# Performance work log

Hardware: AMD Instinct MI355X
Metric: run time of the kernel (lower is better)

The kernel has to match this reference:

```python
import jax, jax.numpy as jnp
import numpy as np

T, F, H = 65536, 128, 64

def setup_inputs() -> dict:
    key = jax.random.key(0)
    ks = jax.random.split(key, 16)
    s1 = 1.0 / np.sqrt(H).astype(np.float32)   # torch nn.LSTM init bound (hidden=64)
    s2 = 1.0 / np.sqrt(F).astype(np.float32)   # torch nn.LSTM(feats, feats) / Linear bound
    u = lambda k, shape, s: jax.random.uniform(k, shape, jnp.float32, -s, s)
    return {
        "x": jax.random.normal(ks[0], (T, F), jnp.float32),
        "h1_0": jax.random.uniform(ks[1], (H,), jnp.float32),   # torch.rand
        "c1_0": jax.random.normal(ks[2], (H,), jnp.float32),    # torch.randn
        "h2_0": jax.random.uniform(ks[3], (F,), jnp.float32),
        "c2_0": jax.random.normal(ks[4], (F,), jnp.float32),
        "W_ih1": u(ks[5], (4 * H, F), s1),
        "W_hh1": u(ks[6], (4 * H, H), s1),
        "b_ih1": u(ks[7], (4 * H,), s1),
        "b_hh1": u(ks[8], (4 * H,), s1),
        "W_ih2": u(ks[9], (4 * F, F), s2),
        "W_hh2": u(ks[10], (4 * F, F), s2),
        "b_ih2": u(ks[11], (4 * F,), s2),
        "b_hh2": u(ks[12], (4 * F,), s2),
        "W_fc": u(ks[13], (F, F), s2),
        "b_fc": u(ks[14], (F,), s2),
    }

def _lstm_cell(gates, h, c, W_hh):
    # gates: precomputed x-part [4D]; torch gate order: i, f, g, o
    g = gates + W_hh @ h
    i, f, gg, o = jnp.split(g, 4)
    c_new = jax.nn.sigmoid(f) * c + jax.nn.sigmoid(i) * jnp.tanh(gg)
    h_new = jax.nn.sigmoid(o) * jnp.tanh(c_new)
    return h_new, c_new

def reference(x, h1_0, c1_0, h2_0, c2_0, W_ih1, W_hh1, b_ih1, b_hh1,
              W_ih2, W_hh2, b_ih2, b_hh2, W_fc, b_fc):
    # Hoist all input-to-hidden GEMMs out of the scan (one big matmul each).
    gx1 = x @ W_ih1.T + (b_ih1 + b_hh1)  # [T, 4H]
    gx2 = x @ W_ih2.T + (b_ih2 + b_hh2)  # [T, 4F]

    def step(carry, gs):
        h1, c1, h2, c2 = carry
        g1, g2 = gs
        h1, c1 = _lstm_cell(g1, h1, c1, W_hh1)  # lstm1: state evolves, output unused
        h2, c2 = _lstm_cell(g2, h2, c2, W_hh2)
        out = 2.0 * jax.nn.sigmoid(W_fc @ h2 + b_fc)
        return (h1, c1, h2, c2), out

    _, ys = jax.lax.scan(step, (h1_0, c1_0, h2_0, c2_0), (gx1, gx2))
    return ys  # [T, F]
```

## Files before the change

### kernel.cpp

```cpp
#include <hip/hip_runtime.h>
#include <hip/hip_fp16.h>

#define T_LEN 65536
#define FDIM  128
#define CH    16
#define SEG   256
#define WARM  128
#define NBLK  (T_LEN / SEG)
#define GXT   256
#define FCT   256

typedef int iv4 __attribute__((ext_vector_type(4)));
typedef _Float16 h8f __attribute__((ext_vector_type(8)));
typedef float f4v __attribute__((ext_vector_type(4)));

__device__ __forceinline__ float frcp(float x) { return __builtin_amdgcn_rcpf(x); }
#define LOG2E 1.4426950408889634f
__device__ __forceinline__ float sigmoid_f(float x) {
  return frcp(1.f + __builtin_amdgcn_exp2f(-LOG2E * x));
}

union G2u { uint2 u2; __half h[4]; };

#define LDS_BARRIER() asm volatile("s_waitcnt lgkmcnt(0)\n\ts_barrier" ::: "memory")

__device__ __forceinline__ h8f cvt8(const float4 lo, const float4 hi) {
  h8f f;
  f[0] = (_Float16)lo.x; f[1] = (_Float16)lo.y;
  f[2] = (_Float16)lo.z; f[3] = (_Float16)lo.w;
  f[4] = (_Float16)hi.x; f[5] = (_Float16)hi.y;
  f[6] = (_Float16)hi.z; f[7] = (_Float16)hi.w;
  return f;
}

__global__ __launch_bounds__(256)
void prep_kernel(const float* __restrict__ Whh2, signed char* __restrict__ qW,
                 float* __restrict__ qscale)
{
  const int row = blockIdx.x * 256 + threadIdx.x;
  const float* wr = Whh2 + (size_t)row * FDIM;
  float mjg[4];
#pragma unroll
  for (int jg = 0; jg < 4; ++jg) {
    float m = 0.f;
#pragma unroll
    for (int kc = 0; kc < 2; ++kc)
#pragma unroll
      for (int j = 0; j < 16; ++j)
        m = fmaxf(m, fabsf(wr[16 * jg + 64 * kc + j]));
    mjg[jg] = m;
  }
  float s = fmaxf(fmaxf(mjg[0], mjg[1]), fmaxf(mjg[2], mjg[3]));
  s = fmaxf(s, 1e-20f);
  qscale[row] = s * (1.f / 16129.f);
  const float inv = 127.f / s;
  signed char* qr = qW + (size_t)row * FDIM;
#pragma unroll
  for (int k = 0; k < FDIM; ++k) {
    int qv = (int)rintf(wr[k] * inv);
    qv = qv < -127 ? -127 : (qv > 127 ? 127 : qv);
    qr[k] = (signed char)qv;
  }
}

__global__ __launch_bounds__(256)
void gx_kernel(const float* __restrict__ x, const float* __restrict__ Wih2,
               const float* __restrict__ bih2, const float* __restrict__ bhh2,
               __half* __restrict__ gx)
{
  __shared__ __align__(16) float  xs[16 * 132];
  __shared__ __align__(16) __half gp[4][16 * 130];

  const int tid  = threadIdx.x;
  const int lane = tid & 63;
  const int w    = tid >> 6;
  const int col  = lane & 15;
  const int kg   = lane >> 4;

  h8f  bf[8][4];
  float bias[8];
  const float gmul = (w == 2) ? (-2.f * LOG2E) : (-LOG2E);
#pragma unroll
  for (int nt = 0; nt < 8; ++nt) {
    const int row = w * 128 + nt * 16 + col;
    bias[nt] = bih2[row] + bhh2[row];
    const float* wr = Wih2 + (size_t)row * FDIM + kg * 8;
#pragma unroll
    for (int kc = 0; kc < 4; ++kc)
      bf[nt][kc] = cvt8(*(const float4*)(wr + kc * 32),
                        *(const float4*)(wr + kc * 32 + 4));
  }

  const int tbase = blockIdx.x * GXT;
  float4 pf0, pf1;
  {
    const int r0 = tid >> 5, c0 = (tid & 31) * 4;
    const int r1 = (256 + tid) >> 5, c1 = ((256 + tid) & 31) * 4;
    pf0 = *(const float4*)(x + (size_t)(tbase + r0) * FDIM + c0);
    pf1 = *(const float4*)(x + (size_t)(tbase + r1) * FDIM + c1);
  }

  for (int tt = 0; tt < GXT; tt += 16) {
    __syncthreads();
    {
      const int r0 = tid >> 5, c0 = (tid & 31) * 4;
      const int r1 = (256 + tid) >> 5, c1 = ((256 + tid) & 31) * 4;
      *(float4*)&xs[r0 * 132 + c0] = pf0;
      *(float4*)&xs[r1 * 132 + c1] = pf1;
    }
    __syncthreads();

    {
      const int ntt = (tt + 16 < GXT) ? (tt + 16) : 0;
      const int r0 = tid >> 5, c0 = (tid & 31) * 4;
      const int r1 = (256 + tid) >> 5, c1 = ((256 + tid) & 31) * 4;
      pf0 = *(const float4*)(x + (size_t)(tbase + ntt + r0) * FDIM + c0);
      pf1 = *(const float4*)(x + (size_t)(tbase + ntt + r1) * FDIM + c1);
    }

    h8f af[4];
#pragma unroll
    for (int kc = 0; kc < 4; ++kc) {
      const float* xr = &xs[col * 132 + kg * 8 + kc * 32];
      af[kc] = cvt8(*(const float4*)xr, *(const float4*)(xr + 4));
    }

#pragma unroll
    for (int nt = 0; nt < 8; ++nt) {
      f4v acc = {0.f, 0.f, 0.f, 0.f};
#pragma unroll
      for (int kc = 0; kc < 4; ++kc)
        acc = __builtin_amdgcn_mfma_f32_16x16x32_f16(af[kc], bf[nt][kc], acc, 0, 0, 0);
#pragma unroll
      for (int j = 0; j < 4; ++j)
        gp[w][(kg * 4 + j) * 130 + nt * 16 + col] =
            __float2half((acc[j] + bias[nt]) * gmul);
    }
    __syncthreads();

#pragma unroll
    for (int i = 0; i < 8; ++i) {
      const int idx = i * 256 + tid;
      const int t = idx >> 7, u = idx & 127;
      const unsigned short hi_ = __half_as_ushort(gp[0][t * 130 + u]);
      const unsigned short hf  = __half_as_ushort(gp[1][t * 130 + u]);
      const unsigned short hg  = __half_as_ushort(gp[2][t * 130 + u]);
      const unsigned short ho  = __half_as_ushort(gp[3][t * 130 + u]);
      uint2 o;
      o.x = (unsigned)hi_ | ((unsigned)hf << 16);
      o.y = (unsigned)hg  | ((unsigned)ho << 16);
      *(uint2*)(gx + ((size_t)(tbase + tt + t) * FDIM + u) * 4) = o;
    }
  }
}

__global__ __launch_bounds__(256)
void scan_kernel(const __half* __restrict__ gx, const signed char* __restrict__ qW,
                 const float* __restrict__ qscale,
                 const float* __restrict__ h20, const float* __restrict__ c20,
                 float* __restrict__ hist)
{
  __shared__ __align__(16) signed char hq[2][FDIM];
  __shared__ __align__(16) char  gxl[2][CH * 1024];
  __shared__ __align__(16) float histb[2][CH * FDIM];

  const int tid  = threadIdx.x;
  const int lane = tid & 63;
  const int wave = tid >> 6;
  const int n    = lane & 15;
  const int jg   = lane >> 4;
  const int X    = jg & 1;
  const int ul   = lane & 31;
  const int u    = 32 * wave + ul;

  const int seg0     = blockIdx.x * SEG;
  const int t0       = (seg0 >= WARM) ? (seg0 - WARM) : 0;
  const int nsteps   = seg0 + SEG - t0;
  const int warm_len = seg0 - t0;

  iv4 bq[2][4][2];
#pragma unroll
  for (int Xc = 0; Xc < 2; ++Xc) {
    const int urow = 32 * wave + 16 * Xc + n;
#pragma unroll
    for (int g = 0; g < 4; ++g) {
      const signed char* qr = qW + (size_t)(g * FDIM + urow) * FDIM + 16 * jg;
#pragma unroll
      for (int kc = 0; kc < 2; ++kc)
        bq[Xc][g][kc] = *(const iv4*)(qr + 64 * kc);
    }
  }
  const float gmul[4] = { -LOG2E, -LOG2E, -2.f * LOG2E, -LOG2E };
  float scl[4];
#pragma unroll
  for (int g = 0; g < 4; ++g) scl[g] = qscale[g * FDIM + u] * gmul[g];

  float c;
  if (blockIdx.x == 0) {
    c = c20[u];
    if (tid < FDIM) {
      const float hv = fminf(fmaxf(h20[tid], -1.f), 1.f);
      hq[0][tid] = (signed char)(int)rintf(127.f * hv);
    }
  } else {
    c = 0.f;
    if (tid < FDIM) hq[0][tid] = 0;
  }

  const uint4* gglob = (const uint4*)gx;
  {
    const uint4* gsrc = gglob + (size_t)(t0 / CH) * 1024;
#pragma unroll
    for (int r = 0; r < 4; ++r) {
      const uint4 v = gsrc[r * 256 + tid];
      *(uint4*)(&gxl[0][r * 4096 + tid * 16]) = v;
    }
  }

  const iv4 zero = {0, 0, 0, 0};
  __syncthreads();

  for (int t4 = 0; t4 < nsteps; t4 += CH) {
    const int chunk = t4 >> 4;
    const int buf   = chunk & 1;

    const int nchunk = ((t0 + t4) / CH + 1) & (T_LEN / CH - 1);
    const uint4 pf0 = gglob[(size_t)nchunk * 1024 + 0 * 256 + tid];
    const uint4 pf1 = gglob[(size_t)nchunk * 1024 + 1 * 256 + tid];
    const uint4 pf2 = gglob[(size_t)nchunk * 1024 + 2 * 256 + tid];
    const uint4 pf3 = gglob[(size_t)nchunk * 1024 + 3 * 256 + tid];

    if (t4 != 0 && (t4 - CH) >= warm_len) {
      float* gdst = hist + (size_t)(t0 + t4 - CH) * FDIM;
      const float* hsb = &histb[1 - buf][0];
#pragma unroll
      for (int j = 0; j < 2; ++j) {
        const float4 v = *(const float4*)(hsb + 4 * (tid + 256 * j));
        *(float4*)(gdst + 4 * (tid + 256 * j)) = v;
      }
    }

#pragma unroll
    for (int s = 0; s < CH; ++s) {
      const signed char* hrow = hq[s & 1];
      const iv4 a0 = *(const iv4*)(hrow + jg * 16);
      const iv4 a1 = *(const iv4*)(hrow + 64 + jg * 16);
      G2u gg; gg.u2 = *(const uint2*)(&gxl[buf][s * 1024 + u * 8]);

      iv4 acc[2][4];
      {
        iv4 d00 = __builtin_amdgcn_mfma_i32_16x16x64_i8(a0, bq[0][0][0], zero, 0, 0, 0);
        iv4 d02 = __builtin_amdgcn_mfma_i32_16x16x64_i8(a0, bq[0][2][0], zero, 0, 0, 0);
        iv4 d10 = __builtin_amdgcn_mfma_i32_16x16x64_i8(a0, bq[1][0][0], zero, 0, 0, 0);
        iv4 d12 = __builtin_amdgcn_mfma_i32_16x16x64_i8(a0, bq[1][2][0], zero, 0, 0, 0);
        acc[0][0] = __builtin_amdgcn_mfma_i32_16x16x64_i8(a1, bq[0][0][1], d00, 0, 0, 0);
        acc[0][2] = __builtin_amdgcn_mfma_i32_16x16x64_i8(a1, bq[0][2][1], d02, 0, 0, 0);
        acc[1][0] = __builtin_amdgcn_mfma_i32_16x16x64_i8(a1, bq[1][0][1], d10, 0, 0, 0);
        acc[1][2] = __builtin_amdgcn_mfma_i32_16x16x64_i8(a1, bq[1][2][1], d12, 0, 0, 0);
      }
      {
        iv4 d01 = __builtin_amdgcn_mfma_i32_16x16x64_i8(a0, bq[0][1][0], zero, 0, 0, 0);
        iv4 d03 = __builtin_amdgcn_mfma_i32_16x16x64_i8(a0, bq[0][3][0], zero, 0, 0, 0);
        iv4 d11 = __builtin_amdgcn_mfma_i32_16x16x64_i8(a0, bq[1][1][0], zero, 0, 0, 0);
        iv4 d13 = __builtin_amdgcn_mfma_i32_16x16x64_i8(a0, bq[1][3][0], zero, 0, 0, 0);
        acc[0][1] = __builtin_amdgcn_mfma_i32_16x16x64_i8(a1, bq[0][1][1], d01, 0, 0, 0);
        acc[0][3] = __builtin_amdgcn_mfma_i32_16x16x64_i8(a1, bq[0][3][1], d03, 0, 0, 0);
        acc[1][1] = __builtin_amdgcn_mfma_i32_16x16x64_i8(a1, bq[1][1][1], d11, 0, 0, 0);
        acc[1][3] = __builtin_amdgcn_mfma_i32_16x16x64_i8(a1, bq[1][3][1], d13, 0, 0, 0);
      }

      float dv[4];
#pragma unroll
      for (int g = 0; g < 4; ++g)
        dv[g] = (float)(X ? acc[1][g][0] : acc[0][g][0]);

      const float ai = fmaf(dv[0], scl[0], __half2float(gg.h[0]));
      const float af = fmaf(dv[1], scl[1], __half2float(gg.h[1]));
      const float ag = fmaf(dv[2], scl[2], __half2float(gg.h[2]));
      const float ao = fmaf(dv[3], scl[3], __half2float(gg.h[3]));

      const float si = frcp(1.f + __builtin_amdgcn_exp2f(ai));
      const float tg = fmaf(frcp(1.f + __builtin_amdgcn_exp2f(ag)), 2.f, -1.f);
      const float sf = frcp(1.f + __builtin_amdgcn_exp2f(af));
      const float so = frcp(1.f + __builtin_amdgcn_exp2f(ao));

      c = fmaf(sf, c, si * tg);
      const float tc = fmaf(frcp(1.f + __builtin_amdgcn_exp2f(-2.f * LOG2E * c)),
                            2.f, -1.f);
      const float h = so * tc;

      hq[(s + 1) & 1][u] = (signed char)(int)rintf(127.f * h);
      histb[buf][s * FDIM + u] = h;

      if (s == CH - 1) {
        *(uint4*)(&gxl[1 - buf][0 * 4096 + tid * 16]) = pf0;
        *(uint4*)(&gxl[1 - buf][1 * 4096 + tid * 16]) = pf1;
        *(uint4*)(&gxl[1 - buf][2 * 4096 + tid * 16]) = pf2;
        *(uint4*)(&gxl[1 - buf][3 * 4096 + tid * 16]) = pf3;
      }
      LDS_BARRIER();
    }
  }

  {
    const int lastbuf = ((nsteps / CH) - 1) & 1;
    float* gdst = hist + (size_t)(t0 + nsteps - CH) * FDIM;
    const float* hsb = &histb[lastbuf][0];
#pragma unroll
    for (int j = 0; j < 2; ++j) {
      const float4 v = *(const float4*)(hsb + 4 * (tid + 256 * j));
      *(float4*)(gdst + 4 * (tid + 256 * j)) = v;
    }
  }
}

__global__ __launch_bounds__(256)
void fc_kernel(const float* __restrict__ Wfc, const float* __restrict__ bfc,
               float* __restrict__ io)
{
  __shared__ __align__(16) float xs[16 * 132];
  __shared__ __align__(16) float os[16 * 132];

  const int tid  = threadIdx.x;
  const int lane = tid & 63;
  const int w    = tid >> 6;
  const int col  = lane & 15;
  const int kg   = lane >> 4;

  h8f  bf[2][4];
  float bias[2];
#pragma unroll
  for (int nt = 0; nt < 2; ++nt) {
    const int row = w * 32 + nt * 16 + col;
    bias[nt] = bfc[row];
    const float* wr = Wfc + (size_t)row * FDIM + kg * 8;
#pragma unroll
    for (int kc = 0; kc < 4; ++kc)
      bf[nt][kc] = cvt8(*(const float4*)(wr + kc * 32),
                        *(const float4*)(wr + kc * 32 + 4));
  }

  const int tbase = blockIdx.x * FCT;
  float4 pf0, pf1;
  {
    const int r0 = tid >> 5, c0 = (tid & 31) * 4;
    const int r1 = (256 + tid) >> 5, c1 = ((256 + tid) & 31) * 4;
    pf0 = *(const float4*)(io + (size_t)(tbase + r0) * FDIM + c0);
    pf1 = *(const float4*)(io + (size_t)(tbase + r1) * FDIM + c1);
  }

  for (int tt = 0; tt < FCT; tt += 16) {
    __syncthreads();
    {
      const int r0 = tid >> 5, c0 = (tid & 31) * 4;
      const int r1 = (256 + tid) >> 5, c1 = ((256 + tid) & 31) * 4;
      *(float4*)&xs[r0 * 132 + c0] = pf0;
      *(float4*)&xs[r1 * 132 + c1] = pf1;
    }
    __syncthreads();

    {
      const int ntt = (tt + 16 < FCT) ? (tt + 16) : 0;
      const int r0 = tid >> 5, c0 = (tid & 31) * 4;
      const int r1 = (256 + tid) >> 5, c1 = ((256 + tid) & 31) * 4;
      pf0 = *(const float4*)(io + (size_t)(tbase + ntt + r0) * FDIM + c0);
      pf1 = *(const float4*)(io + (size_t)(tbase + ntt + r1) * FDIM + c1);
    }

    h8f af[4];
#pragma unroll
    for (int kc = 0; kc < 4; ++kc) {
      const float* xr = &xs[col * 132 + kg * 8 + kc * 32];
      af[kc] = cvt8(*(const float4*)xr, *(const float4*)(xr + 4));
    }

#pragma unroll
    for (int nt = 0; nt < 2; ++nt) {
      f4v acc = {0.f, 0.f, 0.f, 0.f};
#pragma unroll
      for (int kc = 0; kc < 4; ++kc)
        acc = __builtin_amdgcn_mfma_f32_16x16x32_f16(af[kc], bf[nt][kc], acc, 0, 0, 0);
#pragma unroll
      for (int j = 0; j < 4; ++j)
        os[(kg * 4 + j) * 132 + w * 32 + nt * 16 + col] =
            2.f * sigmoid_f(acc[j] + bias[nt]);
    }
    __syncthreads();

#pragma unroll
    for (int i = 0; i < 2; ++i) {
      const int idx = i * 256 + tid;
      const int r = idx >> 5, cidx = (idx & 31) * 4;
      *(float4*)(io + (size_t)(tbase + tt + r) * FDIM + cidx) =
          *(const float4*)&os[r * 132 + cidx];
    }
  }
}

extern "C" void kernel_launch(void* const* d_in, const int* in_sizes, int n_in,
                              void* d_out, int out_size, void* d_ws, size_t ws_size,
                              hipStream_t stream) {
  const float* x    = (const float*)d_in[0];
  const float* h20  = (const float*)d_in[3];
  const float* c20  = (const float*)d_in[4];
  const float* Wih2 = (const float*)d_in[9];
  const float* Whh2 = (const float*)d_in[10];
  const float* bih2 = (const float*)d_in[11];
  const float* bhh2 = (const float*)d_in[12];
  const float* Wfc  = (const float*)d_in[13];
  const float* bfc  = (const float*)d_in[14];

  float*  out = (float*)d_out;
  __half* gx  = (__half*)d_ws;
  signed char* qW = (signed char*)d_ws + (size_t)T_LEN * 1024;
  float* qscale   = (float*)((char*)d_ws + (size_t)T_LEN * 1024 + 512 * FDIM);

  prep_kernel<<<2, 256, 0, stream>>>(Whh2, qW, qscale);
  gx_kernel<<<T_LEN / GXT, 256, 0, stream>>>(x, Wih2, bih2, bhh2, gx);
  scan_kernel<<<NBLK, 256, 0, stream>>>(gx, qW, qscale, h20, c20, out);
  fc_kernel<<<T_LEN / FCT, 256, 0, stream>>>(Wfc, bfc, out);
}
```

Baseline: 287.2 us.

## Fuse input-gate GEMM and FC output layer into the segmented scan kernel

```diff
diff --git a/kernel.cpp b/kernel.cpp
--- a/kernel.cpp
+++ b/kernel.cpp
@@ -7,8 +7,6 @@
 #define SEG   256
 #define WARM  128
 #define NBLK  (T_LEN / SEG)
-#define GXT   256
-#define FCT   256
 
 typedef int iv4 __attribute__((ext_vector_type(4)));
 typedef _Float16 h8f __attribute__((ext_vector_type(8)));
@@ -63,106 +61,21 @@
   }
 }
 
-__global__ __launch_bounds__(256)
-void gx_kernel(const float* __restrict__ x, const float* __restrict__ Wih2,
-               const float* __restrict__ bih2, const float* __restrict__ bhh2,
-               __half* __restrict__ gx)
-{
-  __shared__ __align__(16) float  xs[16 * 132];
-  __shared__ __align__(16) __half gp[4][16 * 130];
-
-  const int tid  = threadIdx.x;
-  const int lane = tid & 63;
-  const int w    = tid >> 6;
-  const int col  = lane & 15;
-  const int kg   = lane >> 4;
-
-  h8f  bf[8][4];
-  float bias[8];
-  const float gmul = (w == 2) ? (-2.f * LOG2E) : (-LOG2E);
-#pragma unroll
-  for (int nt = 0; nt < 8; ++nt) {
-    const int row = w * 128 + nt * 16 + col;
-    bias[nt] = bih2[row] + bhh2[row];
-    const float* wr = Wih2 + (size_t)row * FDIM + kg * 8;
-#pragma unroll
-    for (int kc = 0; kc < 4; ++kc)
-      bf[nt][kc] = cvt8(*(const float4*)(wr + kc * 32),
-                        *(const float4*)(wr + kc * 32 + 4));
-  }
-
-  const int tbase = blockIdx.x * GXT;
-  float4 pf0, pf1;
-  {
-    const int r0 = tid >> 5, c0 = (tid & 31) * 4;
-    const int r1 = (256 + tid) >> 5, c1 = ((256 + tid) & 31) * 4;
-    pf0 = *(const float4*)(x + (size_t)(tbase + r0) * FDIM + c0);
-    pf1 = *(const float4*)(x + (size_t)(tbase + r1) * FDIM + c1);
-  }
-
-  for (int tt = 0; tt < GXT; tt += 16) {
-    __syncthreads();
-    {
-      const int r0 = tid >> 5, c0 = (tid & 31) * 4;
-      const int r1 = (256 + tid) >> 5, c1 = ((256 + tid) & 31) * 4;
-      *(float4*)&xs[r0 * 132 + c0] = pf0;
-      *(float4*)&xs[r1 * 132 + c1] = pf1;
-    }
-    __syncthreads();
-
-    {
-      const int ntt = (tt + 16 < GXT) ? (tt + 16) : 0;
-      const int r0 = tid >> 5, c0 = (tid & 31) * 4;
-      const int r1 = (256 + tid) >> 5, c1 = ((256 + tid) & 31) * 4;
-      pf0 = *(const float4*)(x + (size_t)(tbase + ntt + r0) * FDIM + c0);
-      pf1 = *(const float4*)(x + (size_t)(tbase + ntt + r1) * FDIM + c1);
-    }
-
-    h8f af[4];
-#pragma unroll
-    for (int kc = 0; kc < 4; ++kc) {
-      const float* xr = &xs[col * 132 + kg * 8 + kc * 32];
-      af[kc] = cvt8(*(const float4*)xr, *(const float4*)(xr + 4));
-    }
-
-#pragma unroll
-    for (int nt = 0; nt < 8; ++nt) {
-      f4v acc = {0.f, 0.f, 0.f, 0.f};
-#pragma unroll
-      for (int kc = 0; kc < 4; ++kc)
-        acc = __builtin_amdgcn_mfma_f32_16x16x32_f16(af[kc], bf[nt][kc], acc, 0, 0, 0);
-#pragma unroll
-      for (int j = 0; j < 4; ++j)
-        gp[w][(kg * 4 + j) * 130 + nt * 16 + col] =
-            __float2half((acc[j] + bias[nt]) * gmul);
-    }
-    __syncthreads();
-
-#pragma unroll
-    for (int i = 0; i < 8; ++i) {
-      const int idx = i * 256 + tid;
-      const int t = idx >> 7, u = idx & 127;
-      const unsigned short hi_ = __half_as_ushort(gp[0][t * 130 + u]);
-      const unsigned short hf  = __half_as_ushort(gp[1][t * 130 + u]);
-      const unsigned short hg  = __half_as_ushort(gp[2][t * 130 + u]);
-      const unsigned short ho  = __half_as_ushort(gp[3][t * 130 + u]);
-      uint2 o;
-      o.x = (unsigned)hi_ | ((unsigned)hf << 16);
-      o.y = (unsigned)hg  | ((unsigned)ho << 16);
-      *(uint2*)(gx + ((size_t)(tbase + tt + t) * FDIM + u) * 4) = o;
-    }
-  }
-}
-
-__global__ __launch_bounds__(256)
-void scan_kernel(const __half* __restrict__ gx, const signed char* __restrict__ qW,
+__global__ __launch_bounds__(256, 1)
+void scan_kernel(const float* __restrict__ x,
+                 const signed char* __restrict__ qW,
                  const float* __restrict__ qscale,
+                 const float* __restrict__ Wih2,
+                 const float* __restrict__ bih2, const float* __restrict__ bhh2,
+                 const float* __restrict__ Wfc, const float* __restrict__ bfc,
                  const float* __restrict__ h20, const float* __restrict__ c20,
-                 float* __restrict__ hist)
+                 float* __restrict__ out)
 {
   __shared__ __align__(16) signed char hq[2][FDIM];
   __shared__ __align__(16) char  gxl[2][CH * 1024];
-  __shared__ __align__(16) float histb[2][CH * FDIM];
+  __shared__ __align__(16) float histb[CH * 132];
+  __shared__ __align__(16) float xs[16 * 132];
+  __shared__ __align__(16) float os[16 * 132];
 
   const int tid  = threadIdx.x;
   const int lane = tid & 63;
@@ -177,6 +90,7 @@
   const int t0       = (seg0 >= WARM) ? (seg0 - WARM) : 0;
   const int nsteps   = seg0 + SEG - t0;
   const int warm_len = seg0 - t0;
+  const int nch      = nsteps / CH;
 
   iv4 bq[2][4][2];
 #pragma unroll
@@ -194,6 +108,33 @@
   float scl[4];
 #pragma unroll
   for (int g = 0; g < 4; ++g) scl[g] = qscale[g * FDIM + u] * gmul[g];
+
+  h8f  bf_ih[8][4];
+  float bias_ih[8];
+  const float gmul_w = (wave == 2) ? (-2.f * LOG2E) : (-LOG2E);
+#pragma unroll
+  for (int nt = 0; nt < 8; ++nt) {
+    const int row = wave * 128 + nt * 16 + n;
+    bias_ih[nt] = bih2[row] + bhh2[row];
+    const float* wr = Wih2 + (size_t)row * FDIM + jg * 8;
+#pragma unroll
+    for (int kc = 0; kc < 4; ++kc)
+      bf_ih[nt][kc] = cvt8(*(const float4*)(wr + kc * 32),
+                           *(const float4*)(wr + kc * 32 + 4));
+  }
+
+  h8f  bf_fc[2][4];
+  float bias_fc[2];
+#pragma unroll
+  for (int nt = 0; nt < 2; ++nt) {
+    const int row = wave * 32 + nt * 16 + n;
+    bias_fc[nt] = bfc[row];
+    const float* wr = Wfc + (size_t)row * FDIM + jg * 8;
+#pragma unroll
+    for (int kc = 0; kc < 4; ++kc)
+      bf_fc[nt][kc] = cvt8(*(const float4*)(wr + kc * 32),
+                           *(const float4*)(wr + kc * 32 + 4));
+  }
 
   float c;
   if (blockIdx.x == 0) {
@@ -207,38 +148,55 @@
     if (tid < FDIM) hq[0][tid] = 0;
   }
 
-  const uint4* gglob = (const uint4*)gx;
+  float4 pf0, pf1;
   {
-    const uint4* gsrc = gglob + (size_t)(t0 / CH) * 1024;
-#pragma unroll
-    for (int r = 0; r < 4; ++r) {
-      const uint4 v = gsrc[r * 256 + tid];
-      *(uint4*)(&gxl[0][r * 4096 + tid * 16]) = v;
-    }
+    const int i0 = tid, i1 = 256 + tid;
+    pf0 = *(const float4*)(x + (size_t)(t0 + (i0 >> 5)) * FDIM + (i0 & 31) * 4);
+    pf1 = *(const float4*)(x + (size_t)(t0 + (i1 >> 5)) * FDIM + (i1 & 31) * 4);
   }
 
   const iv4 zero = {0, 0, 0, 0};
   __syncthreads();
 
-  for (int t4 = 0; t4 < nsteps; t4 += CH) {
-    const int chunk = t4 >> 4;
-    const int buf   = chunk & 1;
-
-    const int nchunk = ((t0 + t4) / CH + 1) & (T_LEN / CH - 1);
-    const uint4 pf0 = gglob[(size_t)nchunk * 1024 + 0 * 256 + tid];
-    const uint4 pf1 = gglob[(size_t)nchunk * 1024 + 1 * 256 + tid];
-    const uint4 pf2 = gglob[(size_t)nchunk * 1024 + 2 * 256 + tid];
-    const uint4 pf3 = gglob[(size_t)nchunk * 1024 + 3 * 256 + tid];
-
-    if (t4 != 0 && (t4 - CH) >= warm_len) {
-      float* gdst = hist + (size_t)(t0 + t4 - CH) * FDIM;
-      const float* hsb = &histb[1 - buf][0];
-#pragma unroll
-      for (int j = 0; j < 2; ++j) {
-        const float4 v = *(const float4*)(hsb + 4 * (tid + 256 * j));
-        *(float4*)(gdst + 4 * (tid + 256 * j)) = v;
-      }
-    }
+#define G_PHASE(DST, TPREF)                                                  \
+  {                                                                          \
+    {                                                                        \
+      const int i0 = tid, i1 = 256 + tid;                                    \
+      *(float4*)&xs[(i0 >> 5) * 132 + (i0 & 31) * 4] = pf0;                  \
+      *(float4*)&xs[(i1 >> 5) * 132 + (i1 & 31) * 4] = pf1;                  \
+    }                                                                        \
+    __syncthreads();                                                         \
+    h8f ax[4];                                                               \
+    _Pragma("unroll")                                                        \
+    for (int kc = 0; kc < 4; ++kc) {                                         \
+      const float* xr = &xs[n * 132 + jg * 8 + kc * 32];                     \
+      ax[kc] = cvt8(*(const float4*)xr, *(const float4*)(xr + 4));           \
+    }                                                                        \
+    _Pragma("unroll")                                                        \
+    for (int nt = 0; nt < 8; ++nt) {                                         \
+      f4v acc = {0.f, 0.f, 0.f, 0.f};                                        \
+      _Pragma("unroll")                                                      \
+      for (int kc = 0; kc < 4; ++kc)                                         \
+        acc = __builtin_amdgcn_mfma_f32_16x16x32_f16(ax[kc], bf_ih[nt][kc], acc, 0, 0, 0); \
+      _Pragma("unroll")                                                      \
+      for (int j = 0; j < 4; ++j)                                            \
+        *(__half*)(&gxl[DST][(jg * 4 + j) * 1024 + (nt * 16 + n) * 8 + wave * 2]) = \
+            __float2half((acc[j] + bias_ih[nt]) * gmul_w);                   \
+    }                                                                        \
+    {                                                                        \
+      const int tp = (TPREF) > (T_LEN - CH) ? (T_LEN - CH) : (TPREF);        \
+      const int i0 = tid, i1 = 256 + tid;                                    \
+      pf0 = *(const float4*)(x + (size_t)(tp + (i0 >> 5)) * FDIM + (i0 & 31) * 4); \
+      pf1 = *(const float4*)(x + (size_t)(tp + (i1 >> 5)) * FDIM + (i1 & 31) * 4); \
+    }                                                                        \
+    LDS_BARRIER();                                                           \
+  }
+
+  G_PHASE(0, t0 + CH)
+
+  for (int ci = 0; ci < nch; ++ci) {
+    const int buf = ci & 1;
+    const int t4  = ci * CH;
 
 #pragma unroll
     for (int s = 0; s < CH; ++s) {
@@ -290,111 +248,45 @@
       const float h = so * tc;
 
       hq[(s + 1) & 1][u] = (signed char)(int)rintf(127.f * h);
-      histb[buf][s * FDIM + u] = h;
-
-      if (s == CH - 1) {
-        *(uint4*)(&gxl[1 - buf][0 * 4096 + tid * 16]) = pf0;
-        *(uint4*)(&gxl[1 - buf][1 * 4096 + tid * 16]) = pf1;
-        *(uint4*)(&gxl[1 - buf][2 * 4096 + tid * 16]) = pf2;
-        *(uint4*)(&gxl[1 - buf][3 * 4096 + tid * 16]) = pf3;
-      }
+      histb[s * 132 + u] = h;
       LDS_BARRIER();
     }
-  }
-
-  {
-    const int lastbuf = ((nsteps / CH) - 1) & 1;
-    float* gdst = hist + (size_t)(t0 + nsteps - CH) * FDIM;
-    const float* hsb = &histb[lastbuf][0];
-#pragma unroll
-    for (int j = 0; j < 2; ++j) {
-      const float4 v = *(const float4*)(hsb + 4 * (tid + 256 * j));
-      *(float4*)(gdst + 4 * (tid + 256 * j)) = v;
-    }
-  }
-}
-
-__global__ __launch_bounds__(256)
-void fc_kernel(const float* __restrict__ Wfc, const float* __restrict__ bfc,
-               float* __restrict__ io)
-{
-  __shared__ __align__(16) float xs[16 * 132];
-  __shared__ __align__(16) float os[16 * 132];
-
-  const int tid  = threadIdx.x;
-  const int lane = tid & 63;
-  const int w    = tid >> 6;
-  const int col  = lane & 15;
-  const int kg   = lane >> 4;
-
-  h8f  bf[2][4];
-  float bias[2];
-#pragma unroll
-  for (int nt = 0; nt < 2; ++nt) {
-    const int row = w * 32 + nt * 16 + col;
-    bias[nt] = bfc[row];
-    const float* wr = Wfc + (size_t)row * FDIM + kg * 8;
-#pragma unroll
-    for (int kc = 0; kc < 4; ++kc)
-      bf[nt][kc] = cvt8(*(const float4*)(wr + kc * 32),
-                        *(const float4*)(wr + kc * 32 + 4));
-  }
-
-  const int tbase = blockIdx.x * FCT;
-  float4 pf0, pf1;
-  {
-    const int r0 = tid >> 5, c0 = (tid & 31) * 4;
-    const int r1 = (256 + tid) >> 5, c1 = ((256 + tid) & 31) * 4;
-    pf0 = *(const float4*)(io + (size_t)(tbase + r0) * FDIM + c0);
-    pf1 = *(const float4*)(io + (size_t)(tbase + r1) * FDIM + c1);
-  }
-
-  for (int tt = 0; tt < FCT; tt += 16) {
-    __syncthreads();
+
     {
-      const int r0 = tid >> 5, c0 = (tid & 31) * 4;
-      const int r1 = (256 + tid) >> 5, c1 = ((256 + tid) & 31) * 4;
-      *(float4*)&xs[r0 * 132 + c0] = pf0;
-      *(float4*)&xs[r1 * 132 + c1] = pf1;
-    }
-    __syncthreads();
-
-    {
-      const int ntt = (tt + 16 < FCT) ? (tt + 16) : 0;
-      const int r0 = tid >> 5, c0 = (tid & 31) * 4;
-      const int r1 = (256 + tid) >> 5, c1 = ((256 + tid) & 31) * 4;
-      pf0 = *(const float4*)(io + (size_t)(tbase + ntt + r0) * FDIM + c0);
-      pf1 = *(const float4*)(io + (size_t)(tbase + ntt + r1) * FDIM + c1);
-    }
-
-    h8f af[4];
-#pragma unroll
-    for (int kc = 0; kc < 4; ++kc) {
-      const float* xr = &xs[col * 132 + kg * 8 + kc * 32];
-      af[kc] = cvt8(*(const float4*)xr, *(const float4*)(xr + 4));
-    }
-
-#pragma unroll
-    for (int nt = 0; nt < 2; ++nt) {
-      f4v acc = {0.f, 0.f, 0.f, 0.f};
-#pragma unroll
-      for (int kc = 0; kc < 4; ++kc)
-        acc = __builtin_amdgcn_mfma_f32_16x16x32_f16(af[kc], bf[nt][kc], acc, 0, 0, 0);
-#pragma unroll
-      for (int j = 0; j < 4; ++j)
-        os[(kg * 4 + j) * 132 + w * 32 + nt * 16 + col] =
-            2.f * sigmoid_f(acc[j] + bias[nt]);
-    }
-    __syncthreads();
-
-#pragma unroll
-    for (int i = 0; i < 2; ++i) {
-      const int idx = i * 256 + tid;
-      const int r = idx >> 5, cidx = (idx & 31) * 4;
-      *(float4*)(io + (size_t)(tbase + tt + r) * FDIM + cidx) =
-          *(const float4*)&os[r * 132 + cidx];
-    }
-  }
+      h8f ah[4];
+#pragma unroll
+      for (int kc = 0; kc < 4; ++kc) {
+        const float* hr = &histb[n * 132 + jg * 8 + kc * 32];
+        ah[kc] = cvt8(*(const float4*)hr, *(const float4*)(hr + 4));
+      }
+#pragma unroll
+      for (int nt = 0; nt < 2; ++nt) {
+        f4v acc = {0.f, 0.f, 0.f, 0.f};
+#pragma unroll
+        for (int kc = 0; kc < 4; ++kc)
+          acc = __builtin_amdgcn_mfma_f32_16x16x32_f16(ah[kc], bf_fc[nt][kc], acc, 0, 0, 0);
+#pragma unroll
+        for (int j = 0; j < 4; ++j)
+          os[(jg * 4 + j) * 132 + wave * 32 + nt * 16 + n] =
+              2.f * sigmoid_f(acc[j] + bias_fc[nt]);
+      }
+      LDS_BARRIER();
+      if (t4 >= warm_len) {
+        float* gdst = out + (size_t)(t0 + t4) * FDIM;
+#pragma unroll
+        for (int i = 0; i < 2; ++i) {
+          const int idx = i * 256 + tid;
+          const int r = idx >> 5, cc = (idx & 31) * 4;
+          *(float4*)(gdst + (size_t)r * FDIM + cc) = *(const float4*)&os[r * 132 + cc];
+        }
+      }
+    }
+
+    if (ci + 1 < nch) {
+      G_PHASE(1 - buf, t0 + (ci + 2) * CH)
+    }
+  }
+#undef G_PHASE
 }
 
 extern "C" void kernel_launch(void* const* d_in, const int* in_sizes, int n_in,
@@ -410,13 +302,11 @@
   const float* Wfc  = (const float*)d_in[13];
   const float* bfc  = (const float*)d_in[14];
 
-  float*  out = (float*)d_out;
-  __half* gx  = (__half*)d_ws;
-  signed char* qW = (signed char*)d_ws + (size_t)T_LEN * 1024;
-  float* qscale   = (float*)((char*)d_ws + (size_t)T_LEN * 1024 + 512 * FDIM);
+  float* out = (float*)d_out;
+  signed char* qW = (signed char*)d_ws;
+  float* qscale   = (float*)((char*)d_ws + 512 * FDIM);
 
   prep_kernel<<<2, 256, 0, stream>>>(Whh2, qW, qscale);
-  gx_kernel<<<T_LEN / GXT, 256, 0, stream>>>(x, Wih2, bih2, bhh2, gx);
-  scan_kernel<<<NBLK, 256, 0, stream>>>(gx, qW, qscale, h20, c20, out);
-  fc_kernel<<<T_LEN / FCT, 256, 0, stream>>>(Wfc, bfc, out);
-}
+  scan_kernel<<<NBLK, 256, 0, stream>>>(x, qW, qscale, Wih2, bih2, bhh2,
+                                        Wfc, bfc, h20, c20, out);
+}
```

After: 276.2 us. 1.04x faster.
